# Kernel optimization log

Measured on AMD Instinct MI355X. Metric: run time of the kernel, lower is better.

## Reference

```python
import jax, jax.numpy as jnp
import numpy as np
from jax import lax


def setup_inputs() -> dict:
    key = jax.random.key(0)
    k1, k2, k3, k4, k5 = jax.random.split(key, 5)
    B, T, D, N = 64, 1024, 512, 24
    return {
        "x": jax.random.normal(k1, (B, T, D), dtype=jnp.float32),
        "W": jax.random.normal(k2, (D, N), dtype=jnp.float32) * 0.05,
        "b": jnp.zeros((N,), dtype=jnp.float32),
        "trans": jax.random.normal(k3, (N, N), dtype=jnp.float32) * 0.1,
        "left_boundary": jax.random.normal(k4, (N,), dtype=jnp.float32) * 0.1,
        "right_boundary": jax.random.normal(k5, (N,), dtype=jnp.float32) * 0.1,
    }


def reference(x, W, b, trans, left_boundary, right_boundary):
    # Dense projection to tag potentials: [B, T, N]
    pot = jnp.einsum("btd,dn->btn", x, W) + b
    B, T, N = pot.shape
    # mask=None -> lengths are all T; boundaries added at t=0 and t=T-1
    lens = jnp.full((B,), T, dtype=jnp.int32)
    pot = pot.at[:, 0, :].add(left_boundary).at[:, T - 1, :].add(right_boundary)

    # Viterbi forward: alpha[b, j] = best score of any path ending in tag j
    def fwd_step(alpha, pot_t):
        scores = alpha[:, :, None] + trans[None, :, :]  # [B, prev, cur]
        bp = jnp.argmax(scores, axis=1)                 # [B, N] best prev tag
        alpha_new = jnp.max(scores, axis=1) + pot_t
        return alpha_new, bp

    alpha0 = pot[:, 0, :]
    pot_rest = jnp.swapaxes(pot[:, 1:, :], 0, 1)  # [T-1, B, N]
    alpha_T, bps = lax.scan(fwd_step, alpha0, pot_rest)
    last_tag = jnp.argmax(alpha_T, axis=-1)  # [B]

    # Backtrack through backpointers (reverse scan over time)
    def back_step(tag, bp_t):
        prev = jnp.take_along_axis(bp_t, tag[:, None], axis=1)[:, 0]
        return prev, prev

    _, tags_head = lax.scan(back_step, last_tag, bps, reverse=True)  # [T-1, B]
    decoded = jnp.concatenate(
        [jnp.swapaxes(tags_head, 0, 1), last_tag[:, None]], axis=1
    ).astype(jnp.int32)  # [B, T]
    return decoded, pot, lens, trans
```

## Files before the change

### kernel.cpp

```cpp
#include <hip/hip_runtime.h>
#include <hip/hip_bf16.h>

#define BB 64
#define TT 1024
#define DD 512
#define NS 24

#define POT_OFF   65536
#define LENS_OFF  1638400
#define TRANS_OFF 1638464

__global__ __launch_bounds__(256) void gemm_pot(
    const float* __restrict__ x, const float* __restrict__ W,
    const float* __restrict__ bias, const float* __restrict__ trans,
    const float* __restrict__ lb, const float* __restrict__ rb,
    float* __restrict__ out)
{
  __shared__ float wl[DD * NS];
  const int tid = threadIdx.x;
  const int l   = tid & 63;
  const int q   = tid >> 6;
  const int row = blockIdx.x * 64 + l;

  {
    const float4* Ws = (const float4*)W;
    float4* Wd = (float4*)wl;
#pragma unroll
    for (int i = 0; i < 12; ++i) Wd[tid + i * 256] = Ws[tid + i * 256];
  }
  __syncthreads();

  const float4* xp = (const float4*)(x + (size_t)row * DD + q * 128);

  float acc[NS];
#pragma unroll
  for (int nn = 0; nn < NS; ++nn) acc[nn] = 0.f;

  float4 buf[8];
#pragma unroll
  for (int i = 0; i < 8; ++i) buf[i] = xp[i];

#pragma unroll
  for (int f = 0; f < 32; ++f) {
    float4 v = buf[f & 7];
    if (f + 8 < 32) buf[f & 7] = xp[f + 8];
    const float xj[4] = {v.x, v.y, v.z, v.w};
#pragma unroll
    for (int j = 0; j < 4; ++j) {
      const int k = q * 128 + f * 4 + j;
      const float4* wr = (const float4*)&wl[k * NS];
      float4 w0 = wr[0], w1 = wr[1], w2 = wr[2], w3 = wr[3], w4 = wr[4], w5 = wr[5];
      const float wv[NS] = {w0.x,w0.y,w0.z,w0.w, w1.x,w1.y,w1.z,w1.w,
                            w2.x,w2.y,w2.z,w2.w, w3.x,w3.y,w3.z,w3.w,
                            w4.x,w4.y,w4.z,w4.w, w5.x,w5.y,w5.z,w5.w};
      const float xv = xj[j];
#pragma unroll
      for (int nn = 0; nn < NS; ++nn) acc[nn] = fmaf(xv, wv[nn], acc[nn]);
    }
  }

  __syncthreads();
  if (q != 0) {
#pragma unroll
    for (int nn = 0; nn < NS; ++nn) wl[((q - 1) * 64 + l) * 25 + nn] = acc[nn];
  }
  __syncthreads();
  if (q == 0) {
    const int t = row & (TT - 1);
#pragma unroll
    for (int nn = 0; nn < NS; ++nn)
      acc[nn] += wl[(0 * 64 + l) * 25 + nn] + wl[(1 * 64 + l) * 25 + nn]
               + wl[(2 * 64 + l) * 25 + nn] + bias[nn];
    if (t == 0) {
#pragma unroll
      for (int nn = 0; nn < NS; ++nn) acc[nn] += lb[nn];
    }
    if (t == TT - 1) {
#pragma unroll
      for (int nn = 0; nn < NS; ++nn) acc[nn] += rb[nn];
    }
    float* po = out + POT_OFF + (size_t)row * NS;
#pragma unroll
    for (int i = 0; i < 6; ++i)
      *(float4*)(po + i * 4) = make_float4(acc[4*i], acc[4*i+1], acc[4*i+2], acc[4*i+3]);
  }

  if (blockIdx.x == 0 && tid < BB) out[LENS_OFF + tid] = (float)TT;
  if (blockIdx.x == 1) {
    for (int i = tid; i < NS * NS; i += 256) out[TRANS_OFF + i] = trans[i];
  }
}

__device__ __forceinline__ float m3(float a, float b, float c) {
  return fmaxf(fmaxf(a, b), c);
}

__global__ __launch_bounds__(1024) void viterbi_fused(
    const float* __restrict__ pot, const float* __restrict__ trans,
    float* __restrict__ out_dec)
{
  __shared__ float ps[(TT + 8) * NS];
  __shared__ unsigned char bl[TT * NS];
  __shared__ float tl[NS * NS];
  __shared__ int H[32][NS];
  __shared__ int e[32];

  const int b = blockIdx.x, tid = threadIdx.x;

  {
    const float4* src = (const float4*)(pot + (size_t)b * TT * NS);
    float4* dst = (float4*)ps;
#pragma unroll
    for (int i = 0; i < 6; ++i) dst[tid + i * 1024] = src[tid + i * 1024];
    if (tid < NS * NS) tl[tid] = trans[tid];
  }
  __syncthreads();

  if (tid < 64) {
    const int n = (tid < 24) ? tid : 23;

    float tc[NS];
#pragma unroll
    for (int m = 0; m < NS; ++m) tc[m] = tl[m * NS + n];

    float a_own = ps[n];
    float sal[NS];
#pragma unroll
    for (int m = 0; m < NS; ++m)
      sal[m] = __int_as_float(__builtin_amdgcn_readlane(__float_as_int(a_own), m));

    float pv[8];
#pragma unroll
    for (int u = 0; u < 8; ++u) pv[u] = ps[(1 + u) * NS + n];

    auto step = [&](int tt, float potv) {
      float sc[NS];
#pragma unroll
      for (int m = 0; m < NS; ++m) sc[m] = sal[m] + tc[m];
      float v0 = m3(sc[0],  sc[1],  sc[2]);
      float v1 = m3(sc[3],  sc[4],  sc[5]);
      float v2 = m3(sc[6],  sc[7],  sc[8]);
      float v3 = m3(sc[9],  sc[10], sc[11]);
      float v4 = m3(sc[12], sc[13], sc[14]);
      float v5 = m3(sc[15], sc[16], sc[17]);
      float v6 = m3(sc[18], sc[19], sc[20]);
      float v7 = m3(sc[21], sc[22], sc[23]);
      float w0 = m3(v0, v1, v2);
      float w1 = m3(v3, v4, v5);
      float w2 = fmaxf(v6, v7);
      float pm = m3(w0, w1, w2);
      float anew = pm + potv;
      ps[tt * NS + n] = anew;
#pragma unroll
      for (int m = 0; m < NS; ++m)
        sal[m] = __int_as_float(__builtin_amdgcn_readlane(__float_as_int(anew), m));
    };

    for (int t = 1; t + 7 <= TT - 1; t += 8) {
#pragma unroll
      for (int u = 0; u < 8; ++u) {
        const int tt = t + u;
        const float potv = pv[u];
        pv[u] = ps[(tt + 8) * NS + n];
        step(tt, potv);
      }
    }
#pragma unroll
    for (int u = 0; u < 7; ++u) step(1017 + u, pv[u]);
  }
  __syncthreads();

  for (int idx = tid; idx < (TT - 1) * NS; idx += 1024) {
    const int n = idx % NS;
    const int t = idx / NS + 1;
    const float* ar = &ps[(t - 1) * NS];
    float best = ar[0] + tl[n];
    int bi = 0;
#pragma unroll
    for (int m = 1; m < NS; ++m) {
      float s = ar[m] + tl[m * NS + n];
      bool g = s > best;
      bi = g ? m : bi;
      best = g ? s : best;
    }
    bl[t * NS + n] = (unsigned char)bi;
  }
  __syncthreads();

  if (tid < 32 * NS) {
    const int c = tid / NS, s = tid % NS;
    int a = s;
    int tlo = c * 32; if (tlo < 1) tlo = 1;
    for (int t = c * 32 + 31; t >= tlo; --t) a = bl[t * NS + a];
    H[c][s] = a;
  }
  __syncthreads();

  if (tid == 0) {
    const float* ar = &ps[(TT - 1) * NS];
    float best = ar[0]; int bi = 0;
#pragma unroll
    for (int nn = 1; nn < NS; ++nn) {
      float v = ar[nn];
      if (v > best) { best = v; bi = nn; }
    }
    int tag = bi;
    e[31] = tag;
    for (int c = 31; c >= 1; --c) { tag = H[c][tag]; e[c - 1] = tag; }
  }
  __syncthreads();

  if (tid < 32) {
    const int c = tid;
    int tag = e[c];
    float* od = out_dec + (size_t)b * TT;
    od[c * 32 + 31] = (float)tag;
    for (int t = c * 32 + 30; t >= c * 32; --t) {
      tag = bl[(t + 1) * NS + tag];
      od[t] = (float)tag;
    }
  }
}

extern "C" void kernel_launch(void* const* d_in, const int* in_sizes, int n_in,
                              void* d_out, int out_size, void* d_ws, size_t ws_size,
                              hipStream_t stream)
{
  const float* x     = (const float*)d_in[0];
  const float* W     = (const float*)d_in[1];
  const float* bias  = (const float*)d_in[2];
  const float* trans = (const float*)d_in[3];
  const float* lb    = (const float*)d_in[4];
  const float* rb    = (const float*)d_in[5];
  float* out = (float*)d_out;

  gemm_pot<<<1024, 256, 0, stream>>>(x, W, bias, trans, lb, rb, out);
  viterbi_fused<<<BB, 1024, 0, stream>>>(out + POT_OFF, trans, out);
}
```

Measured before the change: 349.2 us.

## Split Viterbi max-reduction across wave lanes using DPP rotates and permlane swaps

Restructures the serial Viterbi forward recurrence so that each step's 24-way max over previous tags is split across two lane groups of 16 candidates each. The two halves are combined with permlane32_swap, and the new alpha is rebroadcast with permlane16_swap plus DPP row rotates instead of 24 readlane instructions. This shortens the per-step dependency chain, which dominates the single-wave sequential loop, at the cost of more cross-lane ops and padded lanes holding -inf entries. The remaining edits rename variables to avoid shadowing.

```diff
diff --git a/kernel.cpp b/kernel.cpp
--- a/kernel.cpp
+++ b/kernel.cpp
@@ -95,6 +95,9 @@
   return fmaxf(fmaxf(a, b), c);
 }
 
+#define RORI(dst, src, J) \
+  dst = __builtin_amdgcn_mov_dpp((src), 0x120 + (J), 0xF, 0xF, true)
+
 __global__ __launch_bounds__(1024) void viterbi_fused(
     const float* __restrict__ pot, const float* __restrict__ trans,
     float* __restrict__ out_dec)
@@ -117,43 +120,79 @@
   __syncthreads();
 
   if (tid < 64) {
-    const int n = (tid < 24) ? tid : 23;
-
-    float tc[NS];
-#pragma unroll
-    for (int m = 0; m < NS; ++m) tc[m] = tl[m * NS + n];
-
-    float a_own = ps[n];
-    float sal[NS];
-#pragma unroll
-    for (int m = 0; m < NS; ++m)
-      sal[m] = __int_as_float(__builtin_amdgcn_readlane(__float_as_int(a_own), m));
+    const int r = tid >> 4;
+    const int c = tid & 15;
+    const int g = r >> 1;
+    const int n = 16 * (r & 1) + c;
+    const int nm = (n < NS) ? n : (NS - 1);
+    const bool wr = (n < NS) && (g == 0);
+
+    int colv[16];
+    colv[0] = c;
+    RORI(colv[1],  c, 1);  RORI(colv[2],  c, 2);  RORI(colv[3],  c, 3);
+    RORI(colv[4],  c, 4);  RORI(colv[5],  c, 5);  RORI(colv[6],  c, 6);
+    RORI(colv[7],  c, 7);  RORI(colv[8],  c, 8);  RORI(colv[9],  c, 9);
+    RORI(colv[10], c, 10); RORI(colv[11], c, 11); RORI(colv[12], c, 12);
+    RORI(colv[13], c, 13); RORI(colv[14], c, 14); RORI(colv[15], c, 15);
+
+    bool selx;
+    {
+      auto nr = __builtin_amdgcn_permlane16_swap(n, n, false, false);
+      selx = (nr[0] == 16 * g + c);
+    }
+
+    float tcr[16];
+#pragma unroll
+    for (int j = 0; j < 16; ++j) {
+      const int m = 16 * g + colv[j];
+      tcr[j] = (m < NS) ? tl[m * NS + nm] : -__builtin_inff();
+    }
+
+    float ar[16];
+#pragma unroll
+    for (int j = 0; j < 16; ++j) {
+      const int m = 16 * g + colv[j];
+      ar[j] = ps[(m < NS) ? m : (NS - 1)];
+    }
 
     float pv[8];
 #pragma unroll
-    for (int u = 0; u < 8; ++u) pv[u] = ps[(1 + u) * NS + n];
+    for (int u = 0; u < 8; ++u) pv[u] = ps[(1 + u) * NS + nm];
 
     auto step = [&](int tt, float potv) {
-      float sc[NS];
-#pragma unroll
-      for (int m = 0; m < NS; ++m) sc[m] = sal[m] + tc[m];
-      float v0 = m3(sc[0],  sc[1],  sc[2]);
-      float v1 = m3(sc[3],  sc[4],  sc[5]);
-      float v2 = m3(sc[6],  sc[7],  sc[8]);
-      float v3 = m3(sc[9],  sc[10], sc[11]);
-      float v4 = m3(sc[12], sc[13], sc[14]);
-      float v5 = m3(sc[15], sc[16], sc[17]);
-      float v6 = m3(sc[18], sc[19], sc[20]);
-      float v7 = m3(sc[21], sc[22], sc[23]);
-      float w0 = m3(v0, v1, v2);
-      float w1 = m3(v3, v4, v5);
-      float w2 = fmaxf(v6, v7);
-      float pm = m3(w0, w1, w2);
-      float anew = pm + potv;
-      ps[tt * NS + n] = anew;
-#pragma unroll
-      for (int m = 0; m < NS; ++m)
-        sal[m] = __int_as_float(__builtin_amdgcn_readlane(__float_as_int(anew), m));
+      float sc[16];
+#pragma unroll
+      for (int j = 0; j < 16; ++j) sc[j] = ar[j] + tcr[j];
+      float u0 = m3(sc[0],  sc[1],  sc[2]);
+      float u1 = m3(sc[3],  sc[4],  sc[5]);
+      float u2 = m3(sc[6],  sc[7],  sc[8]);
+      float u3 = m3(sc[9],  sc[10], sc[11]);
+      float u4 = m3(sc[12], sc[13], sc[14]);
+      float pm = fmaxf(m3(u0, u1, u2), m3(u3, u4, sc[15]));
+      auto pr = __builtin_amdgcn_permlane32_swap(
+          __float_as_int(pm), __float_as_int(pm), false, false);
+      float al = fmaxf(__int_as_float(pr[0]), __int_as_float(pr[1])) + potv;
+      if (wr) ps[tt * NS + n] = al;
+      auto qr = __builtin_amdgcn_permlane16_swap(
+          __float_as_int(al), __float_as_int(al), false, false);
+      int asel = selx ? qr[0] : qr[1];
+      ar[0] = __int_as_float(asel);
+      int d1, d2, d3, d4, d5, d6, d7, d8, d9, d10, d11, d12, d13, d14, d15;
+      RORI(d1,  asel, 1);  ar[1]  = __int_as_float(d1);
+      RORI(d2,  asel, 2);  ar[2]  = __int_as_float(d2);
+      RORI(d3,  asel, 3);  ar[3]  = __int_as_float(d3);
+      RORI(d4,  asel, 4);  ar[4]  = __int_as_float(d4);
+      RORI(d5,  asel, 5);  ar[5]  = __int_as_float(d5);
+      RORI(d6,  asel, 6);  ar[6]  = __int_as_float(d6);
+      RORI(d7,  asel, 7);  ar[7]  = __int_as_float(d7);
+      RORI(d8,  asel, 8);  ar[8]  = __int_as_float(d8);
+      RORI(d9,  asel, 9);  ar[9]  = __int_as_float(d9);
+      RORI(d10, asel, 10); ar[10] = __int_as_float(d10);
+      RORI(d11, asel, 11); ar[11] = __int_as_float(d11);
+      RORI(d12, asel, 12); ar[12] = __int_as_float(d12);
+      RORI(d13, asel, 13); ar[13] = __int_as_float(d13);
+      RORI(d14, asel, 14); ar[14] = __int_as_float(d14);
+      RORI(d15, asel, 15); ar[15] = __int_as_float(d15);
     };
 
     for (int t = 1; t + 7 <= TT - 1; t += 8) {
@@ -161,7 +200,7 @@
       for (int u = 0; u < 8; ++u) {
         const int tt = t + u;
         const float potv = pv[u];
-        pv[u] = ps[(tt + 8) * NS + n];
+        pv[u] = ps[(tt + 8) * NS + nm];
         step(tt, potv);
       }
     }
@@ -179,20 +218,20 @@
 #pragma unroll
     for (int m = 1; m < NS; ++m) {
       float s = ar[m] + tl[m * NS + n];
-      bool g = s > best;
-      bi = g ? m : bi;
-      best = g ? s : best;
+      bool gg = s > best;
+      bi = gg ? m : bi;
+      best = gg ? s : best;
     }
     bl[t * NS + n] = (unsigned char)bi;
   }
   __syncthreads();
 
   if (tid < 32 * NS) {
-    const int c = tid / NS, s = tid % NS;
-    int a = s;
-    int tlo = c * 32; if (tlo < 1) tlo = 1;
-    for (int t = c * 32 + 31; t >= tlo; --t) a = bl[t * NS + a];
-    H[c][s] = a;
+    const int c2 = tid / NS, s = tid % NS;
+    int a2 = s;
+    int tlo = c2 * 32; if (tlo < 1) tlo = 1;
+    for (int t = c2 * 32 + 31; t >= tlo; --t) a2 = bl[t * NS + a2];
+    H[c2][s] = a2;
   }
   __syncthreads();
 
@@ -206,16 +245,16 @@
     }
     int tag = bi;
     e[31] = tag;
-    for (int c = 31; c >= 1; --c) { tag = H[c][tag]; e[c - 1] = tag; }
+    for (int c2 = 31; c2 >= 1; --c2) { tag = H[c2][tag]; e[c2 - 1] = tag; }
   }
   __syncthreads();
 
   if (tid < 32) {
-    const int c = tid;
-    int tag = e[c];
+    const int c2 = tid;
+    int tag = e[c2];
     float* od = out_dec + (size_t)b * TT;
-    od[c * 32 + 31] = (float)tag;
-    for (int t = c * 32 + 30; t >= c * 32; --t) {
+    od[c2 * 32 + 31] = (float)tag;
+    for (int t = c2 * 32 + 30; t >= c2 * 32; --t) {
       tag = bl[(t + 1) * NS + tag];
       od[t] = (float)tag;
     }
```

Measured after the change: 327.0 us. 6.4% less time.
